# Performance work log

Hardware: AMD Instinct MI355X
Metric: run time of the kernel (lower is better)

The kernel has to match this reference:

```python
import jax, jax.numpy as jnp
import numpy as np

SP_BETA = 1.0       # rendering_options.sp_beta
INF_DELTA = 1e10    # use_inf_depth=True -> last delta is 1e10
EPS = 1e-10


def setup_inputs() -> dict:
    key = jax.random.key(0)
    k1, k2, k3 = jax.random.split(key, 3)
    B, R, S, C = 8, 16384, 64, 3  # batch, rays, samples-per-ray, rgb channels
    colors = jax.random.normal(k1, (B, R, S, C), dtype=jnp.float32)
    densities = jax.random.normal(k2, (B, R, S, 1), dtype=jnp.float32)
    # depths must be sorted (increasing) along the sample dimension
    depths = jnp.sort(
        jax.random.uniform(k3, (B, R, S, 1), dtype=jnp.float32, minval=0.1, maxval=6.0),
        axis=2,
    )
    return {"colors": colors, "densities": densities, "depths": depths}


def reference(colors, densities, depths):
    # deltas between consecutive samples, last delta = 1e10 (infinite far plane)
    deltas = depths[:, :, 1:] - depths[:, :, :-1]                      # [B,R,S-1,1]
    deltas = jnp.concatenate(
        [deltas, jnp.full_like(deltas[:, :, :1], INF_DELTA)], axis=2)  # [B,R,S,1]

    # clamp_mode == 'softplus' with beta=1.0: softplus(x*beta)/beta
    dens = jax.nn.softplus(densities * SP_BETA) / SP_BETA              # [B,R,S,1]

    alphas = 1.0 - jnp.exp(-deltas * dens)                             # [B,R,S,1]

    # transmittance: cumulative product of (1-alpha), with leading ones
    trans = jnp.cumprod(1.0 - alphas + EPS, axis=2)                    # [B,R,S,1]
    trans = jnp.concatenate([jnp.ones_like(trans[:, :, :1]), trans], axis=2)  # [B,R,S+1,1]

    final_transmittance = trans[:, :, -1, 0]                           # [B,R]
    weights = alphas * trans[:, :, :-1]                                # [B,R,S,1]

    rgb_final = (weights * colors).sum(axis=2)                         # [B,R,C]
    depth = (weights * depths).sum(axis=2)                             # [B,R,1]
    return rgb_final, depth, weights, final_transmittance
```

## Files before the change

### kernel.cpp

```cpp
#include <hip/hip_runtime.h>

#define INF_DELTA 1e10f
#define LOG2E 1.4426950408889634f
#define LOG2_EPS -33.219280948873623f

typedef float floatx4 __attribute__((ext_vector_type(4)));

template<int CTRL, int RMASK>
__device__ __forceinline__ float dpp0(float v) {
    return __int_as_float(
        __builtin_amdgcn_update_dpp(0, __float_as_int(v), CTRL, RMASK, 0xF, false));
}

__device__ __forceinline__ float log2_softplus(float x) {
    const float q  = __builtin_amdgcn_exp2f(-__builtin_fabsf(x) * LOG2E);
    const float l2 = __builtin_amdgcn_logf(1.0f + q);
    return __builtin_fmaf(__builtin_fmaxf(x, 0.0f), LOG2E, l2);
}

__global__ __launch_bounds__(256) void raymarch_kernel(
    const float* __restrict__ colors,
    const float* __restrict__ densities,
    const float* __restrict__ depths,
    float* __restrict__ rgb_out,
    float* __restrict__ depth_out,
    float* __restrict__ weights_out,
    float* __restrict__ trans_out,
    int n_rays)
{
    const int lane = threadIdx.x & 63;
    const int wid  = threadIdx.x >> 6;
    const int blk  = blockIdx.x * 4 + wid;
    const int nblk = n_rays >> 2;
    if (blk >= nblk) return;

    const long fbase = (long)blk * 256;

    const float4 d4 = *reinterpret_cast<const float4*>(depths    + fbase + lane * 4);
    const float4 x4 = *reinterpret_cast<const float4*>(densities + fbase + lane * 4);
    const float* cp = colors + fbase * 3 + lane * 12;
    const float4 ca = *reinterpret_cast<const float4*>(cp);
    const float4 cb = *reinterpret_cast<const float4*>(cp + 4);
    const float4 cc = *reinterpret_cast<const float4*>(cp + 8);

    const float dnx  = dpp0<0x101, 0xF>(d4.x);
    const float del0 = d4.y - d4.x;
    const float del1 = d4.z - d4.y;
    const float del2 = d4.w - d4.z;
    const float del3 = ((lane & 15) == 15) ? INF_DELTA : (dnx - d4.w);

    const float g0 = -del0 * log2_softplus(x4.x);
    const float g1 = -del1 * log2_softplus(x4.y);
    const float g2 = -del2 * log2_softplus(x4.z);
    const float g3 = -del3 * log2_softplus(x4.w);
    const float a0 = 1.0f - __builtin_amdgcn_exp2f(g0);
    const float a1 = 1.0f - __builtin_amdgcn_exp2f(g1);
    const float a2 = 1.0f - __builtin_amdgcn_exp2f(g2);
    const float a3 = 1.0f - __builtin_amdgcn_exp2f(g3);
    const float l0 = __builtin_fmaxf(g0, LOG2_EPS);
    const float l1 = __builtin_fmaxf(g1, LOG2_EPS);
    const float l2 = __builtin_fmaxf(g2, LOG2_EPS);
    const float l3 = __builtin_fmaxf(g3, LOG2_EPS);

    const float L0 = l0;
    const float L1 = L0 + l1;
    const float L2 = L1 + l2;
    const float L3 = L2 + l3;
    float p = L3;
    p += dpp0<0x111, 0xF>(p);
    p += dpp0<0x112, 0xF>(p);
    p += dpp0<0x114, 0xF>(p);
    p += dpp0<0x118, 0xF>(p);
    const float excl = p - L3;

    const float e0 = __builtin_amdgcn_exp2f(excl);
    const float e1 = __builtin_amdgcn_exp2f(excl + L0);
    const float e2 = __builtin_amdgcn_exp2f(excl + L1);
    const float e3 = __builtin_amdgcn_exp2f(excl + L2);

    const float w0 = a0 * e0;
    const float w1 = a1 * e1;
    const float w2 = a2 * e2;
    const float w3 = a3 * e3;

    floatx4 wv; wv.x = w0; wv.y = w1; wv.z = w2; wv.w = w3;
    __builtin_nontemporal_store(wv,
        reinterpret_cast<floatx4*>(weights_out + fbase + lane * 4));

    float p0 = w0 * ca.x + w1 * ca.w + w2 * cb.z + w3 * cc.y;
    float p1 = w0 * ca.y + w1 * cb.x + w2 * cb.w + w3 * cc.z;
    float p2 = w0 * ca.z + w1 * cb.y + w2 * cc.x + w3 * cc.w;
    float p3 = w0 * d4.x + w1 * d4.y + w2 * d4.z + w3 * d4.w;

    p0 += dpp0<0xB1, 0xF>(p0);
    p1 += dpp0<0xB1, 0xF>(p1);
    p2 += dpp0<0xB1, 0xF>(p2);
    p3 += dpp0<0xB1, 0xF>(p3);
    p0 += dpp0<0x4E, 0xF>(p0);
    p1 += dpp0<0x4E, 0xF>(p1);
    p2 += dpp0<0x4E, 0xF>(p2);
    p3 += dpp0<0x4E, 0xF>(p3);

    const int c = lane & 15;
    const int sel = lane & 3;
    float v = (sel == 0) ? p0 : (sel == 1) ? p1 : (sel == 2) ? p2 : p3;
    v += dpp0<0x124, 0xF>(v);
    v += dpp0<0x128, 0xF>(v);

    const int ray = blk * 4 + (lane >> 4);
    if (c < 3) {
        __builtin_nontemporal_store(v, rgb_out + (long)ray * 3 + c);
    } else if (c == 3) {
        __builtin_nontemporal_store(v, depth_out + ray);
    }
    if (c == 15) {
        __builtin_nontemporal_store(__builtin_amdgcn_exp2f(p), trans_out + ray);
    }
}

extern "C" void kernel_launch(void* const* d_in, const int* in_sizes, int n_in,
                              void* d_out, int out_size, void* d_ws, size_t ws_size,
                              hipStream_t stream) {
    const float* colors    = (const float*)d_in[0];
    const float* densities = (const float*)d_in[1];
    const float* depths    = (const float*)d_in[2];

    const int n_rays = in_sizes[1] / 64;

    float* out      = (float*)d_out;
    float* rgb      = out;
    float* depth_o  = rgb + (long)n_rays * 3;
    float* weights  = depth_o + n_rays;
    float* trans    = weights + (long)n_rays * 64;

    const int nblk   = n_rays / 4;
    const int blocks = (nblk + 3) / 4;
    raymarch_kernel<<<blocks, 256, 0, stream>>>(
        colors, densities, depths, rgb, depth_o, weights, trans, n_rays);
}
```

Baseline: 202.3 us.

## Use grid-stride persistent waves with software-prefetched next tile loads

Replaces the one-tile-per-wave launch with a fixed grid of 2048 blocks that loop over tiles in grid-stride order. Each iteration issues the loads for the next tile before computing the current one, so memory latency overlaps with the exp/log math and DPP reductions. It also cuts block launch overhead. The cost is more registers per thread for the prefetched values, a redundant reload on the last iteration, and fewer resident waves available to hide latency by oversubscription.

```diff
diff --git a/kernel.cpp b/kernel.cpp
--- a/kernel.cpp
+++ b/kernel.cpp
@@ -30,91 +30,107 @@
 {
     const int lane = threadIdx.x & 63;
     const int wid  = threadIdx.x >> 6;
-    const int blk  = blockIdx.x * 4 + wid;
     const int nblk = n_rays >> 2;
-    if (blk >= nblk) return;
+    const int nw   = gridDim.x * 4;
+    int t = blockIdx.x * 4 + wid;
+    if (t >= nblk) return;
 
-    const long fbase = (long)blk * 256;
+    long fb = (long)t * 256;
+    float4 d4 = *reinterpret_cast<const float4*>(depths    + fb + lane * 4);
+    float4 x4 = *reinterpret_cast<const float4*>(densities + fb + lane * 4);
+    const float* cp0 = colors + fb * 3 + lane * 12;
+    float4 ca = *reinterpret_cast<const float4*>(cp0);
+    float4 cb = *reinterpret_cast<const float4*>(cp0 + 4);
+    float4 cc = *reinterpret_cast<const float4*>(cp0 + 8);
 
-    const float4 d4 = *reinterpret_cast<const float4*>(depths    + fbase + lane * 4);
-    const float4 x4 = *reinterpret_cast<const float4*>(densities + fbase + lane * 4);
-    const float* cp = colors + fbase * 3 + lane * 12;
-    const float4 ca = *reinterpret_cast<const float4*>(cp);
-    const float4 cb = *reinterpret_cast<const float4*>(cp + 4);
-    const float4 cc = *reinterpret_cast<const float4*>(cp + 8);
+    while (t < nblk) {
+        const int  tn  = t + nw;
+        const long fbn = (long)((tn < nblk) ? tn : t) * 256;
+        const float4 d4n = *reinterpret_cast<const float4*>(depths    + fbn + lane * 4);
+        const float4 x4n = *reinterpret_cast<const float4*>(densities + fbn + lane * 4);
+        const float* cpn = colors + fbn * 3 + lane * 12;
+        const float4 can = *reinterpret_cast<const float4*>(cpn);
+        const float4 cbn = *reinterpret_cast<const float4*>(cpn + 4);
+        const float4 ccn = *reinterpret_cast<const float4*>(cpn + 8);
 
-    const float dnx  = dpp0<0x101, 0xF>(d4.x);
-    const float del0 = d4.y - d4.x;
-    const float del1 = d4.z - d4.y;
-    const float del2 = d4.w - d4.z;
-    const float del3 = ((lane & 15) == 15) ? INF_DELTA : (dnx - d4.w);
+        const long fbase = (long)t * 256;
 
-    const float g0 = -del0 * log2_softplus(x4.x);
-    const float g1 = -del1 * log2_softplus(x4.y);
-    const float g2 = -del2 * log2_softplus(x4.z);
-    const float g3 = -del3 * log2_softplus(x4.w);
-    const float a0 = 1.0f - __builtin_amdgcn_exp2f(g0);
-    const float a1 = 1.0f - __builtin_amdgcn_exp2f(g1);
-    const float a2 = 1.0f - __builtin_amdgcn_exp2f(g2);
-    const float a3 = 1.0f - __builtin_amdgcn_exp2f(g3);
-    const float l0 = __builtin_fmaxf(g0, LOG2_EPS);
-    const float l1 = __builtin_fmaxf(g1, LOG2_EPS);
-    const float l2 = __builtin_fmaxf(g2, LOG2_EPS);
-    const float l3 = __builtin_fmaxf(g3, LOG2_EPS);
+        const float dnx  = dpp0<0x101, 0xF>(d4.x);
+        const float del0 = d4.y - d4.x;
+        const float del1 = d4.z - d4.y;
+        const float del2 = d4.w - d4.z;
+        const float del3 = ((lane & 15) == 15) ? INF_DELTA : (dnx - d4.w);
 
-    const float L0 = l0;
-    const float L1 = L0 + l1;
-    const float L2 = L1 + l2;
-    const float L3 = L2 + l3;
-    float p = L3;
-    p += dpp0<0x111, 0xF>(p);
-    p += dpp0<0x112, 0xF>(p);
-    p += dpp0<0x114, 0xF>(p);
-    p += dpp0<0x118, 0xF>(p);
-    const float excl = p - L3;
+        const float g0 = -del0 * log2_softplus(x4.x);
+        const float g1 = -del1 * log2_softplus(x4.y);
+        const float g2 = -del2 * log2_softplus(x4.z);
+        const float g3 = -del3 * log2_softplus(x4.w);
+        const float a0 = 1.0f - __builtin_amdgcn_exp2f(g0);
+        const float a1 = 1.0f - __builtin_amdgcn_exp2f(g1);
+        const float a2 = 1.0f - __builtin_amdgcn_exp2f(g2);
+        const float a3 = 1.0f - __builtin_amdgcn_exp2f(g3);
+        const float l0 = __builtin_fmaxf(g0, LOG2_EPS);
+        const float l1 = __builtin_fmaxf(g1, LOG2_EPS);
+        const float l2 = __builtin_fmaxf(g2, LOG2_EPS);
+        const float l3 = __builtin_fmaxf(g3, LOG2_EPS);
 
-    const float e0 = __builtin_amdgcn_exp2f(excl);
-    const float e1 = __builtin_amdgcn_exp2f(excl + L0);
-    const float e2 = __builtin_amdgcn_exp2f(excl + L1);
-    const float e3 = __builtin_amdgcn_exp2f(excl + L2);
+        const float L0 = l0;
+        const float L1 = L0 + l1;
+        const float L2 = L1 + l2;
+        const float L3 = L2 + l3;
+        float p = L3;
+        p += dpp0<0x111, 0xF>(p);
+        p += dpp0<0x112, 0xF>(p);
+        p += dpp0<0x114, 0xF>(p);
+        p += dpp0<0x118, 0xF>(p);
+        const float excl = p - L3;
 
-    const float w0 = a0 * e0;
-    const float w1 = a1 * e1;
-    const float w2 = a2 * e2;
-    const float w3 = a3 * e3;
+        const float e0 = __builtin_amdgcn_exp2f(excl);
+        const float e1 = __builtin_amdgcn_exp2f(excl + L0);
+        const float e2 = __builtin_amdgcn_exp2f(excl + L1);
+        const float e3 = __builtin_amdgcn_exp2f(excl + L2);
 
-    floatx4 wv; wv.x = w0; wv.y = w1; wv.z = w2; wv.w = w3;
-    __builtin_nontemporal_store(wv,
-        reinterpret_cast<floatx4*>(weights_out + fbase + lane * 4));
+        const float w0 = a0 * e0;
+        const float w1 = a1 * e1;
+        const float w2 = a2 * e2;
+        const float w3 = a3 * e3;
 
-    float p0 = w0 * ca.x + w1 * ca.w + w2 * cb.z + w3 * cc.y;
-    float p1 = w0 * ca.y + w1 * cb.x + w2 * cb.w + w3 * cc.z;
-    float p2 = w0 * ca.z + w1 * cb.y + w2 * cc.x + w3 * cc.w;
-    float p3 = w0 * d4.x + w1 * d4.y + w2 * d4.z + w3 * d4.w;
+        floatx4 wv; wv.x = w0; wv.y = w1; wv.z = w2; wv.w = w3;
+        __builtin_nontemporal_store(wv,
+            reinterpret_cast<floatx4*>(weights_out + fbase + lane * 4));
 
-    p0 += dpp0<0xB1, 0xF>(p0);
-    p1 += dpp0<0xB1, 0xF>(p1);
-    p2 += dpp0<0xB1, 0xF>(p2);
-    p3 += dpp0<0xB1, 0xF>(p3);
-    p0 += dpp0<0x4E, 0xF>(p0);
-    p1 += dpp0<0x4E, 0xF>(p1);
-    p2 += dpp0<0x4E, 0xF>(p2);
-    p3 += dpp0<0x4E, 0xF>(p3);
+        float p0 = w0 * ca.x + w1 * ca.w + w2 * cb.z + w3 * cc.y;
+        float p1 = w0 * ca.y + w1 * cb.x + w2 * cb.w + w3 * cc.z;
+        float p2 = w0 * ca.z + w1 * cb.y + w2 * cc.x + w3 * cc.w;
+        float p3 = w0 * d4.x + w1 * d4.y + w2 * d4.z + w3 * d4.w;
 
-    const int c = lane & 15;
-    const int sel = lane & 3;
-    float v = (sel == 0) ? p0 : (sel == 1) ? p1 : (sel == 2) ? p2 : p3;
-    v += dpp0<0x124, 0xF>(v);
-    v += dpp0<0x128, 0xF>(v);
+        p0 += dpp0<0xB1, 0xF>(p0);
+        p1 += dpp0<0xB1, 0xF>(p1);
+        p2 += dpp0<0xB1, 0xF>(p2);
+        p3 += dpp0<0xB1, 0xF>(p3);
+        p0 += dpp0<0x4E, 0xF>(p0);
+        p1 += dpp0<0x4E, 0xF>(p1);
+        p2 += dpp0<0x4E, 0xF>(p2);
+        p3 += dpp0<0x4E, 0xF>(p3);
 
-    const int ray = blk * 4 + (lane >> 4);
-    if (c < 3) {
-        __builtin_nontemporal_store(v, rgb_out + (long)ray * 3 + c);
-    } else if (c == 3) {
-        __builtin_nontemporal_store(v, depth_out + ray);
-    }
-    if (c == 15) {
-        __builtin_nontemporal_store(__builtin_amdgcn_exp2f(p), trans_out + ray);
+        const int c   = lane & 15;
+        const int sel = lane & 3;
+        float v = (sel == 0) ? p0 : (sel == 1) ? p1 : (sel == 2) ? p2 : p3;
+        v += dpp0<0x124, 0xF>(v);
+        v += dpp0<0x128, 0xF>(v);
+
+        const int ray = t * 4 + (lane >> 4);
+        if (c < 3) {
+            __builtin_nontemporal_store(v, rgb_out + (long)ray * 3 + c);
+        } else if (c == 3) {
+            __builtin_nontemporal_store(v, depth_out + ray);
+        }
+        if (c == 15) {
+            __builtin_nontemporal_store(__builtin_amdgcn_exp2f(p), trans_out + ray);
+        }
+
+        d4 = d4n; x4 = x4n; ca = can; cb = cbn; cc = ccn;
+        t = tn;
     }
 }
 
@@ -133,8 +149,9 @@
     float* weights  = depth_o + n_rays;
     float* trans    = weights + (long)n_rays * 64;
 
-    const int nblk   = n_rays / 4;
-    const int blocks = (nblk + 3) / 4;
+    const int nblk = n_rays / 4;
+    int blocks = 2048;
+    if (blocks > (nblk + 3) / 4) blocks = (nblk + 3) / 4;
     raymarch_kernel<<<blocks, 256, 0, stream>>>(
         colors, densities, depths, rgb, depth_o, weights, trans, n_rays);
 }
```

After: 208.3 us. 3.0% more time.
